# Kernel tuning notes

Measured on AMD Instinct MI355X. Metric: run time of the kernel, lower is better.

The kernel has to match this reference:

```python
import jax, jax.numpy as jnp
import numpy as np

NH = 16
HD = 128
ROPE_THETA = 10000.0


def _rope_tables(L, dtype):
    inv_freq = 1.0 / (ROPE_THETA ** (jnp.arange(0, HD, 2, dtype=jnp.float32) / HD))
    t = jnp.arange(L, dtype=jnp.float32)
    freqs = jnp.outer(t, inv_freq)          # [L, HD/2]
    emb = jnp.concatenate([freqs, freqs], axis=-1)  # [L, HD]
    return jnp.cos(emb).astype(dtype), jnp.sin(emb).astype(dtype)


def _rotate_half(x):
    x1, x2 = jnp.split(x, 2, axis=-1)
    return jnp.concatenate([-x2, x1], axis=-1)


def _apply_rope(x, cos, sin):
    return x * cos + _rotate_half(x) * sin


def setup_inputs() -> dict:
    key = jax.random.key(0)
    k1, k2, k3 = jax.random.split(key, 3)
    B, L, H = 2, 2048, 2048
    x = jax.random.normal(k1, (B, L, H), dtype=jnp.float32)
    w_qkv = jax.random.normal(k2, (3 * H, H), dtype=jnp.float32) * 0.02
    w_o = jax.random.normal(k3, (H, H), dtype=jnp.float32) * 0.02
    return {"x": x, "w_qkv": w_qkv, "w_o": w_o}


def reference(x, w_qkv, w_o):
    B, L, H = x.shape
    qkv = x @ w_qkv.T                                   # [B, L, 3H]
    qkv = qkv.reshape(B, L, 3, NH, HD).transpose(2, 0, 3, 1, 4)  # [3, B, NH, L, HD]
    q, k, v = qkv[0], qkv[1], qkv[2]
    cos, sin = _rope_tables(L, x.dtype)
    cos, sin = cos[None, None], sin[None, None]         # [1, 1, L, HD]
    q = _apply_rope(q, cos, sin)
    k = _apply_rope(k, cos, sin)
    scale = 1.0 / jnp.sqrt(jnp.asarray(HD, dtype=x.dtype))
    scores = jnp.einsum('bhqd,bhkd->bhqk', q, k) * scale
    causal = jnp.tril(jnp.ones((L, L), dtype=bool))
    scores = jnp.where(causal[None, None], scores, jnp.asarray(-1e30, dtype=x.dtype))
    attn = jax.nn.softmax(scores, axis=-1)
    out = jnp.einsum('bhqk,bhkd->bhqd', attn, v)        # [B, NH, L, HD]
    out = out.transpose(0, 2, 1, 3).reshape(B, L, H)
    return out @ w_o.T
```

## Files before the change

kernel.cpp:

```cpp
#include <hip/hip_runtime.h>

#define NHEADS 16
#define HD 128
#define LSEQ 2048
#define NBATCH 2
#define HDIM 2048
#define NQKV 6144
#define SCALE 0.08838834764831845f

typedef __attribute__((ext_vector_type(8))) short bfx8;
typedef __attribute__((ext_vector_type(4))) short bfx4;
typedef __attribute__((ext_vector_type(4))) float f32x4;

__device__ __forceinline__ unsigned short f2bf(float x) {
  unsigned u = __float_as_uint(x);
  u += 0x7fffu + ((u >> 16) & 1u);
  return (unsigned short)(u >> 16);
}
__device__ __forceinline__ float bf2f(unsigned short u) {
  return __uint_as_float(((unsigned)u) << 16);
}
__device__ __forceinline__ void gload_lds16(const void* g, void* l) {
  __builtin_amdgcn_global_load_lds(
      (const __attribute__((address_space(1))) unsigned int*)g,
      (__attribute__((address_space(3))) unsigned int*)l, 16, 0, 0);
}

__global__ __launch_bounds__(256) void cast_bf16_kernel(
    const float* __restrict__ in, unsigned short* __restrict__ out, int n4) {
  int i = blockIdx.x * 256 + threadIdx.x;
  if (i >= n4) return;
  float4 v = ((const float4*)in)[i];
  bfx4 o;
  o[0] = (short)f2bf(v.x);
  o[1] = (short)f2bf(v.y);
  o[2] = (short)f2bf(v.z);
  o[3] = (short)f2bf(v.w);
  ((bfx4*)out)[i] = o;
}

template<bool BF16OUT>
__global__ __launch_bounds__(256) void gemm_bt_kernel(
    const unsigned short* __restrict__ A, const unsigned short* __restrict__ B,
    void* __restrict__ Cout, int M, int N, int K) {
  __shared__ unsigned short lA[128 * 64];
  __shared__ unsigned short lB[128 * 64];
  const int tid = threadIdx.x;
  const int w = tid >> 6, lane = tid & 63;
  const int g = lane >> 4, ln = lane & 15;
  const int bm = blockIdx.x * 128, bn = blockIdx.y * 128;
  const int wm = (w >> 1) * 64, wn = (w & 1) * 64;
  const int srow = lane >> 3;
  const int scol = (lane & 7) * 8;

  f32x4 acc[4][4];
#pragma unroll
  for (int i = 0; i < 4; ++i)
#pragma unroll
    for (int j = 0; j < 4; ++j) acc[i][j] = (f32x4){0.f, 0.f, 0.f, 0.f};

  for (int k0 = 0; k0 < K; k0 += 64) {
#pragma unroll
    for (int p = 0; p < 4; ++p) {
      int seg = p * 4 + w;
      int row = seg * 8 + srow;
      const unsigned short* gA = A + (size_t)(bm + row) * K + (k0 + scol);
      const unsigned short* gB = B + (size_t)(bn + row) * K + (k0 + scol);
      gload_lds16(gA, lA + seg * 512);
      gload_lds16(gB, lB + seg * 512);
    }
    __syncthreads();
#pragma unroll
    for (int kk = 0; kk < 2; ++kk) {
      bfx8 af[4], bfr[4];
#pragma unroll
      for (int i = 0; i < 4; ++i)
        af[i] = *(const bfx8*)(lA + (wm + i * 16 + ln) * 64 + kk * 32 + g * 8);
#pragma unroll
      for (int j = 0; j < 4; ++j)
        bfr[j] = *(const bfx8*)(lB + (wn + j * 16 + ln) * 64 + kk * 32 + g * 8);
#pragma unroll
      for (int i = 0; i < 4; ++i)
#pragma unroll
        for (int j = 0; j < 4; ++j)
          acc[i][j] = __builtin_amdgcn_mfma_f32_16x16x32_bf16(af[i], bfr[j], acc[i][j], 0, 0, 0);
    }
    __syncthreads();
  }
#pragma unroll
  for (int i = 0; i < 4; ++i) {
    int row0 = bm + wm + i * 16 + g * 4;
#pragma unroll
    for (int j = 0; j < 4; ++j) {
      int col = bn + wn + j * 16 + ln;
#pragma unroll
      for (int r = 0; r < 4; ++r) {
        if constexpr (BF16OUT)
          ((unsigned short*)Cout)[(size_t)(row0 + r) * N + col] = f2bf(acc[i][j][r]);
        else
          ((float*)Cout)[(size_t)(row0 + r) * N + col] = acc[i][j][r];
      }
    }
  }
}

__global__ __launch_bounds__(256) void rope_scatter_kernel(
    const unsigned short* __restrict__ qkv,
    unsigned short* __restrict__ Qo, unsigned short* __restrict__ Ko,
    unsigned short* __restrict__ Vt) {
  __shared__ unsigned short lV[32 * 128];
  const int bh = blockIdx.x;
  const int l0 = blockIdx.y * 32;
  const int b = bh >> 4, h = bh & 15;
  const int tid = threadIdx.x;
#pragma unroll
  for (int it = 0; it < 2; ++it) {
    int idx = it * 256 + tid;
    int ll = idx >> 4;
    int dq = idx & 15;
    int l = l0 + ll;
    const unsigned short* row = qkv + (size_t)(b * LSEQ + l) * NQKV + h * HD;
    bfx4 qlo = *(const bfx4*)(row + dq * 4);
    bfx4 qhi = *(const bfx4*)(row + 64 + dq * 4);
    bfx4 klo = *(const bfx4*)(row + 2048 + dq * 4);
    bfx4 khi = *(const bfx4*)(row + 2048 + 64 + dq * 4);
    bfx4 vlo = *(const bfx4*)(row + 4096 + dq * 4);
    bfx4 vhi = *(const bfx4*)(row + 4096 + 64 + dq * 4);
    bfx4 oqlo, oqhi, oklo, okhi;
#pragma unroll
    for (int e = 0; e < 4; ++e) {
      int d2 = dq * 4 + e;
      float invf = exp2f(-(float)d2 * 0.2076205059304601f);
      float fr = (float)l * invf;
      float s, c;
      sincosf(fr, &s, &c);
      float xq1 = bf2f((unsigned short)qlo[e]), xq2 = bf2f((unsigned short)qhi[e]);
      oqlo[e] = (short)f2bf(xq1 * c - xq2 * s);
      oqhi[e] = (short)f2bf(xq2 * c + xq1 * s);
      float xk1 = bf2f((unsigned short)klo[e]), xk2 = bf2f((unsigned short)khi[e]);
      oklo[e] = (short)f2bf(xk1 * c - xk2 * s);
      okhi[e] = (short)f2bf(xk2 * c + xk1 * s);
    }
    size_t obase = ((size_t)bh * LSEQ + l) * HD;
    *(bfx4*)(Qo + obase + dq * 4) = oqlo;
    *(bfx4*)(Qo + obase + 64 + dq * 4) = oqhi;
    *(bfx4*)(Ko + obase + dq * 4) = oklo;
    *(bfx4*)(Ko + obase + 64 + dq * 4) = okhi;
    *(bfx4*)(lV + ll * 128 + dq * 4) = vlo;
    *(bfx4*)(lV + ll * 128 + 64 + dq * 4) = vhi;
  }
  __syncthreads();
#pragma unroll
  for (int it = 0; it < 16; ++it) {
    int idx = it * 256 + tid;
    int d = idx >> 5;
    int ll = idx & 31;
    Vt[((size_t)bh * HD + d) * LSEQ + l0 + ll] = lV[ll * 128 + d];
  }
}

__global__ __launch_bounds__(512, 4) void flash_kernel(
    const unsigned short* __restrict__ Q, const unsigned short* __restrict__ K,
    const unsigned short* __restrict__ Vt, unsigned short* __restrict__ O) {
  __shared__ unsigned short lKs[2][64 * 128];
  __shared__ unsigned short lVs[2][128 * 64];
  __shared__ unsigned short lP[8][16 * 40];
  const int bh = blockIdx.x;
  const int qt = 15 - (int)blockIdx.y;
  const int q0 = qt * 128;
  const int tid = threadIdx.x;
  const int w = tid >> 6, lane = tid & 63;
  const int g = lane >> 4, ln = lane & 15;
  const int q0w = q0 + w * 16;
  const unsigned short* Qb = Q + (size_t)bh * LSEQ * HD;
  const unsigned short* Kb = K + (size_t)bh * LSEQ * HD;
  const unsigned short* Vb = Vt + (size_t)bh * HD * LSEQ;
  unsigned short* Pw = lP[w];

  auto STAGE = [&](int buf, int kv0s) {
#pragma unroll
    for (int s = 0; s < 2; ++s) {
      int rl = s * 32 + w * 4 + (lane >> 4);
      int slot = lane & 15;
      const unsigned short* src =
          Kb + (size_t)(kv0s + rl) * HD + ((slot ^ (rl & 15)) * 8);
      gload_lds16(src, &lKs[buf][(s * 8192 + w * 1024) / 2]);
    }
#pragma unroll
    for (int s = 0; s < 2; ++s) {
      int d = s * 64 + w * 8 + (lane >> 3);
      int slot = lane & 7;
      const unsigned short* src =
          Vb + (size_t)d * LSEQ + kv0s + ((slot ^ (d & 7)) * 8);
      gload_lds16(src, &lVs[buf][(s * 8192 + w * 1024) / 2]);
    }
  };

  bfx8 qf[4];
#pragma unroll
  for (int c = 0; c < 4; ++c)
    qf[c] = *(const bfx8*)(Qb + (size_t)(q0w + ln) * HD + c * 32 + g * 8);

  f32x4 o[8];
#pragma unroll
  for (int dt = 0; dt < 8; ++dt) o[dt] = (f32x4){0.f, 0.f, 0.f, 0.f};
  float m = -1e30f, sum = 0.f;
  const int qg = q0w + ln;
  const int nch = 2 * qt + 2;

  STAGE(0, 0);
  __syncthreads();

  for (int ch = 0; ch < nch; ++ch) {
    const int kv0 = ch * 64;
    const int cur = ch & 1;
    if (ch + 1 < nch) STAGE(cur ^ 1, kv0 + 64);

    if (kv0 <= q0w + 15) {
      const char* lK0 = (const char*)lKs[cur];
      const char* lV0 = (const char*)lVs[cur];
      f32x4 s4[4];
#pragma unroll
      for (int kt = 0; kt < 4; ++kt) s4[kt] = (f32x4){0.f, 0.f, 0.f, 0.f};
#pragma unroll
      for (int c = 0; c < 4; ++c) {
        const int cbb = c * 64 + g * 16;
#pragma unroll
        for (int kt = 0; kt < 4; ++kt) {
          bfx8 kf = *(const bfx8*)(lK0 + (kt * 16 + ln) * 256 + (cbb ^ (ln << 4)));
          s4[kt] = __builtin_amdgcn_mfma_f32_16x16x32_bf16(kf, qf[c], s4[kt], 0, 0, 0);
        }
      }
      float tm = -1e30f;
      if (kv0 + 63 <= q0w) {
#pragma unroll
        for (int kt = 0; kt < 4; ++kt)
#pragma unroll
          for (int r = 0; r < 4; ++r) {
            s4[kt][r] *= SCALE;
            tm = fmaxf(tm, s4[kt][r]);
          }
      } else {
#pragma unroll
        for (int kt = 0; kt < 4; ++kt)
#pragma unroll
          for (int r = 0; r < 4; ++r) {
            int kvr = kv0 + kt * 16 + 4 * g + r;
            float v = (kvr <= qg) ? s4[kt][r] * SCALE : -1e30f;
            s4[kt][r] = v;
            tm = fmaxf(tm, v);
          }
      }
      tm = fmaxf(tm, __shfl_xor(tm, 16));
      tm = fmaxf(tm, __shfl_xor(tm, 32));
      float f = 1.f;
      const bool dorescale = !__all(tm <= m + 8.f);
      if (dorescale) {
        float mnew = fmaxf(m, tm);
        f = __expf(m - mnew);
        m = mnew;
      }
      float ts = 0.f;
      bfx4 pb4[4];
#pragma unroll
      for (int kt = 0; kt < 4; ++kt)
#pragma unroll
        for (int r = 0; r < 4; ++r) {
          float p = __expf(s4[kt][r] - m);
          ts += p;
          pb4[kt][r] = (short)f2bf(p);
        }
      ts += __shfl_xor(ts, 16);
      ts += __shfl_xor(ts, 32);
      sum = sum * f + ts;
      float fr0 = 1.f, fr1 = 1.f, fr2 = 1.f, fr3 = 1.f;
      if (dorescale) {
        fr0 = __shfl(f, 4 * g + 0);
        fr1 = __shfl(f, 4 * g + 1);
        fr2 = __shfl(f, 4 * g + 2);
        fr3 = __shfl(f, 4 * g + 3);
      }
#pragma unroll
      for (int kvh = 0; kvh < 2; ++kvh) {
        asm volatile("s_waitcnt lgkmcnt(0)" ::: "memory");
        __builtin_amdgcn_sched_barrier(0);
        *(bfx4*)(Pw + ln * 40 + 4 * g) = pb4[2 * kvh];
        *(bfx4*)(Pw + ln * 40 + 16 + 4 * g) = pb4[2 * kvh + 1];
        asm volatile("s_waitcnt lgkmcnt(0)" ::: "memory");
        __builtin_amdgcn_sched_barrier(0);
        bfx8 pf = *(const bfx8*)(Pw + ln * 40 + g * 8);
        if (kvh == 0 && dorescale) {
#pragma unroll
          for (int dt = 0; dt < 8; ++dt) {
            o[dt][0] *= fr0; o[dt][1] *= fr1; o[dt][2] *= fr2; o[dt][3] *= fr3;
          }
        }
#pragma unroll
        for (int dt = 0; dt < 8; ++dt) {
          bfx8 vf = *(const bfx8*)(lV0 + (dt * 16 + ln) * 128 +
                                   ((kvh * 64 + g * 16) ^ ((ln & 7) << 4)));
          o[dt] = __builtin_amdgcn_mfma_f32_16x16x32_bf16(pf, vf, o[dt], 0, 0, 0);
        }
      }
    }
    __syncthreads();
  }

  float inv = 1.f / sum;
  float ir0 = __shfl(inv, 4 * g + 0);
  float ir1 = __shfl(inv, 4 * g + 1);
  float ir2 = __shfl(inv, 4 * g + 2);
  float ir3 = __shfl(inv, 4 * g + 3);
  const int b = bh >> 4, h = bh & 15;
  unsigned short* Ob = O + (size_t)b * LSEQ * HDIM + h * HD;
#pragma unroll
  for (int dt = 0; dt < 8; ++dt) {
    Ob[(size_t)(q0w + 4 * g + 0) * HDIM + dt * 16 + ln] = f2bf(o[dt][0] * ir0);
    Ob[(size_t)(q0w + 4 * g + 1) * HDIM + dt * 16 + ln] = f2bf(o[dt][1] * ir1);
    Ob[(size_t)(q0w + 4 * g + 2) * HDIM + dt * 16 + ln] = f2bf(o[dt][2] * ir2);
    Ob[(size_t)(q0w + 4 * g + 3) * HDIM + dt * 16 + ln] = f2bf(o[dt][3] * ir3);
  }
}

extern "C" void kernel_launch(void* const* d_in, const int* in_sizes, int n_in,
                              void* d_out, int out_size, void* d_ws, size_t ws_size,
                              hipStream_t stream) {
  const float* x = (const float*)d_in[0];
  const float* w_qkv = (const float*)d_in[1];
  const float* w_o = (const float*)d_in[2];
  float* out = (float*)d_out;
  char* ws = (char*)d_ws;

  unsigned short* xb    = (unsigned short*)(ws + 0);
  unsigned short* wqkvb = (unsigned short*)(ws + 16777216);
  unsigned short* wob   = (unsigned short*)(ws + 41943040);
  unsigned short* qkvb  = (unsigned short*)(ws + 50331648);
  unsigned short* qb    = (unsigned short*)(ws + 100663296);
  unsigned short* kb    = (unsigned short*)(ws + 117440512);
  unsigned short* vtb   = (unsigned short*)(ws + 134217728);
  unsigned short* attnb = (unsigned short*)(ws + 0);

  cast_bf16_kernel<<<8388608 / 4 / 256, 256, 0, stream>>>(x, xb, 8388608 / 4);
  cast_bf16_kernel<<<12582912 / 4 / 256, 256, 0, stream>>>(w_qkv, wqkvb, 12582912 / 4);
  cast_bf16_kernel<<<4194304 / 4 / 256, 256, 0, stream>>>(w_o, wob, 4194304 / 4);

  gemm_bt_kernel<true><<<dim3(4096 / 128, 6144 / 128), 256, 0, stream>>>(
      xb, wqkvb, (void*)qkvb, 4096, 6144, 2048);

  rope_scatter_kernel<<<dim3(32, 64), 256, 0, stream>>>(qkvb, qb, kb, vtb);

  flash_kernel<<<dim3(32, 16), 512, 0, stream>>>(qb, kb, vtb, attnb);

  gemm_bt_kernel<false><<<dim3(4096 / 128, 2048 / 128), 256, 0, stream>>>(
      attnb, wob, (void*)out, 4096, 2048, 2048);
}
```

Baseline: 314.3 us.

## Add 256x256 double-buffered GEMM kernel with XCD swizzle for QKV projection

Adds a new bf16 GEMM kernel that uses 256x256 output tiles with 512 threads. It double-buffers LDS, loading the next K-slice through direct global-to-LDS copies with an XOR swizzle, and interleaves those loads with MFMA phases under a raised wave priority. Workgroup IDs are remapped so neighbouring tiles land on the same XCD. The QKV projection now uses this kernel to get more operand reuse and hide load latency. In exchange it needs 128 KB of LDS per block and carries high register pressure.

```diff
diff --git a/kernel.cpp b/kernel.cpp
--- a/kernel.cpp
+++ b/kernel.cpp
@@ -37,6 +37,102 @@
   o[2] = (short)f2bf(v.z);
   o[3] = (short)f2bf(v.w);
   ((bfx4*)out)[i] = o;
+}
+
+template<bool BF16OUT>
+__global__ __launch_bounds__(512, 2) void gemm256_kernel(
+    const unsigned short* __restrict__ A, const unsigned short* __restrict__ B,
+    void* __restrict__ Cout, int M, int N, int K) {
+  __shared__ unsigned short lA[2][256 * 64];
+  __shared__ unsigned short lB[2][256 * 64];
+  const int tid = threadIdx.x;
+  const int w = tid >> 6, lane = tid & 63;
+  const int g = lane >> 4, ln = lane & 15;
+  const int nmt = M >> 8, nnt = N >> 8;
+  const int nwg = nmt * nnt;
+  const int bid = blockIdx.x;
+  const int swz = (bid & 7) * (nwg >> 3) + (bid >> 3);
+  const int bm = (swz / nnt) * 256, bn = (swz % nnt) * 256;
+  const int wm = (w >> 2) * 128, wn = (w & 3) * 64;
+
+  auto STAGE = [&](int buf, int k0, int q) {
+    int rid = q * 64 + w * 8 + (lane >> 3);
+    int slot = lane & 7;
+    gload_lds16(A + (size_t)(bm + rid) * K + k0 + ((slot ^ (rid & 7)) << 3),
+                &lA[buf][(q * 512 + w * 64) * 8]);
+    gload_lds16(B + (size_t)(bn + rid) * K + k0 + ((slot ^ (rid & 7)) << 3),
+                &lB[buf][(q * 512 + w * 64) * 8]);
+  };
+
+  f32x4 acc[8][4];
+#pragma unroll
+  for (int i = 0; i < 8; ++i)
+#pragma unroll
+    for (int j = 0; j < 4; ++j) acc[i][j] = (f32x4){0.f, 0.f, 0.f, 0.f};
+
+#pragma unroll
+  for (int q = 0; q < 4; ++q) STAGE(0, 0, q);
+  asm volatile("s_waitcnt vmcnt(0)" ::: "memory");
+  asm volatile("s_barrier" ::: "memory");
+
+  const int nt = K >> 6;
+  for (int t = 0; t < nt; ++t) {
+    const int cur = t & 1;
+    const char* lAc = (const char*)lA[cur];
+    const char* lBc = (const char*)lB[cur];
+    const int k0n = (t + 1) << 6;
+    bfx8 bfrag[4][2];
+#pragma unroll
+    for (int ph = 0; ph < 4; ++ph) {
+      if (t + 1 < nt) STAGE(cur ^ 1, k0n, ph);
+      bfx8 afrag[2][2];
+#pragma unroll
+      for (int mi = 0; mi < 2; ++mi)
+#pragma unroll
+        for (int kk = 0; kk < 2; ++kk)
+          afrag[mi][kk] = *(const bfx8*)(lAc + (wm + ph * 32 + mi * 16 + ln) * 128 +
+                                         (((kk * 4 + g) ^ (ln & 7)) << 4));
+      if (ph == 0) {
+#pragma unroll
+        for (int nf = 0; nf < 4; ++nf)
+#pragma unroll
+          for (int kk = 0; kk < 2; ++kk)
+            bfrag[nf][kk] = *(const bfx8*)(lBc + (wn + nf * 16 + ln) * 128 +
+                                           (((kk * 4 + g) ^ (ln & 7)) << 4));
+      }
+      asm volatile("s_waitcnt lgkmcnt(0)" ::: "memory");
+      __builtin_amdgcn_sched_barrier(0);
+      __builtin_amdgcn_s_setprio(1);
+#pragma unroll
+      for (int kk = 0; kk < 2; ++kk)
+#pragma unroll
+        for (int mi = 0; mi < 2; ++mi)
+#pragma unroll
+          for (int nf = 0; nf < 4; ++nf)
+            acc[ph * 2 + mi][nf] = __builtin_amdgcn_mfma_f32_16x16x32_bf16(
+                afrag[mi][kk], bfrag[nf][kk], acc[ph * 2 + mi][nf], 0, 0, 0);
+      __builtin_amdgcn_s_setprio(0);
+      if (ph < 3) asm volatile("s_barrier" ::: "memory");
+    }
+    asm volatile("s_waitcnt vmcnt(0)" ::: "memory");
+    asm volatile("s_barrier" ::: "memory");
+  }
+
+#pragma unroll
+  for (int mf = 0; mf < 8; ++mf) {
+    int row0 = bm + wm + mf * 16 + g * 4;
+#pragma unroll
+    for (int nf = 0; nf < 4; ++nf) {
+      int col = bn + wn + nf * 16 + ln;
+#pragma unroll
+      for (int r = 0; r < 4; ++r) {
+        if constexpr (BF16OUT)
+          ((unsigned short*)Cout)[(size_t)(row0 + r) * N + col] = f2bf(acc[mf][nf][r]);
+        else
+          ((float*)Cout)[(size_t)(row0 + r) * N + col] = acc[mf][nf][r];
+      }
+    }
+  }
 }
 
 template<bool BF16OUT>
@@ -344,7 +440,7 @@
   cast_bf16_kernel<<<12582912 / 4 / 256, 256, 0, stream>>>(w_qkv, wqkvb, 12582912 / 4);
   cast_bf16_kernel<<<4194304 / 4 / 256, 256, 0, stream>>>(w_o, wob, 4194304 / 4);
 
-  gemm_bt_kernel<true><<<dim3(4096 / 128, 6144 / 128), 256, 0, stream>>>(
+  gemm256_kernel<true><<<(4096 / 256) * (6144 / 256), 512, 0, stream>>>(
       xb, wqkvb, (void*)qkvb, 4096, 6144, 2048);
 
   rope_scatter_kernel<<<dim3(32, 64), 256, 0, stream>>>(qkvb, qb, kb, vtb);
```

Measured after the change: 354.7 us. 12.9% more time.

## Replace LDS-staged GEMM with direct global-to-register MFMA loads and swizzled tiles

Applied to the files above, without the earlier changes.

The GEMM kernel no longer stages A/B tiles through shared memory with global_load_lds and barriers. Each wave now loads its MFMA fragments straight from global memory into registers. Blocks are launched on a 1D grid with an XCD-style swizzle of block index to tile, and the QKV projection uses a 128x192 tile. This removes the LDS traffic and __syncthreads stalls, but each row is now fetched redundantly by several waves through L2/L1. Loads are also strided and not coalesced per lane, and with no software prefetch, latency may be exposed.

```diff
diff --git a/kernel.cpp b/kernel.cpp
--- a/kernel.cpp
+++ b/kernel.cpp
@@ -39,66 +39,65 @@
   ((bfx4*)out)[i] = o;
 }
 
-template<bool BF16OUT>
-__global__ __launch_bounds__(256) void gemm_bt_kernel(
+template<int WN, bool BF16OUT>
+__global__ __launch_bounds__(256, 2) void gemm_flat_kernel(
     const unsigned short* __restrict__ A, const unsigned short* __restrict__ B,
     void* __restrict__ Cout, int M, int N, int K) {
-  __shared__ unsigned short lA[128 * 64];
-  __shared__ unsigned short lB[128 * 64];
+  constexpr int NF = WN / 16;
+  constexpr int BN = 2 * WN;
   const int tid = threadIdx.x;
   const int w = tid >> 6, lane = tid & 63;
   const int g = lane >> 4, ln = lane & 15;
-  const int bm = blockIdx.x * 128, bn = blockIdx.y * 128;
-  const int wm = (w >> 1) * 64, wn = (w & 1) * 64;
-  const int srow = lane >> 3;
-  const int scol = (lane & 7) * 8;
-
-  f32x4 acc[4][4];
+  const int nnt = N / BN;
+  const int nwg = (M >> 7) * nnt;
+  const int bid = blockIdx.x;
+  const int swz = (bid & 7) * (nwg >> 3) + (bid >> 3);
+  const int bm = (swz / nnt) * 128, bn = (swz % nnt) * BN;
+  const int rowA = bm + (w >> 1) * 64 + ln;
+  const int colB = bn + (w & 1) * WN + ln;
+  const unsigned short* pA = A + (size_t)rowA * K + g * 8;
+  const unsigned short* pB = B + (size_t)colB * K + g * 8;
+
+  f32x4 acc[4][NF];
 #pragma unroll
   for (int i = 0; i < 4; ++i)
 #pragma unroll
-    for (int j = 0; j < 4; ++j) acc[i][j] = (f32x4){0.f, 0.f, 0.f, 0.f};
+    for (int j = 0; j < NF; ++j) acc[i][j] = (f32x4){0.f, 0.f, 0.f, 0.f};
 
   for (int k0 = 0; k0 < K; k0 += 64) {
-#pragma unroll
-    for (int p = 0; p < 4; ++p) {
-      int seg = p * 4 + w;
-      int row = seg * 8 + srow;
-      const unsigned short* gA = A + (size_t)(bm + row) * K + (k0 + scol);
-      const unsigned short* gB = B + (size_t)(bn + row) * K + (k0 + scol);
-      gload_lds16(gA, lA + seg * 512);
-      gload_lds16(gB, lB + seg * 512);
-    }
-    __syncthreads();
-#pragma unroll
-    for (int kk = 0; kk < 2; ++kk) {
-      bfx8 af[4], bfr[4];
-#pragma unroll
-      for (int i = 0; i < 4; ++i)
-        af[i] = *(const bfx8*)(lA + (wm + i * 16 + ln) * 64 + kk * 32 + g * 8);
-#pragma unroll
-      for (int j = 0; j < 4; ++j)
-        bfr[j] = *(const bfx8*)(lB + (wn + j * 16 + ln) * 64 + kk * 32 + g * 8);
-#pragma unroll
-      for (int i = 0; i < 4; ++i)
-#pragma unroll
-        for (int j = 0; j < 4; ++j)
-          acc[i][j] = __builtin_amdgcn_mfma_f32_16x16x32_bf16(af[i], bfr[j], acc[i][j], 0, 0, 0);
-    }
-    __syncthreads();
-  }
-#pragma unroll
-  for (int i = 0; i < 4; ++i) {
-    int row0 = bm + wm + i * 16 + g * 4;
-#pragma unroll
-    for (int j = 0; j < 4; ++j) {
-      int col = bn + wn + j * 16 + ln;
+    bfx8 a[4][2], b[NF][2];
+#pragma unroll
+    for (int mf = 0; mf < 4; ++mf)
+#pragma unroll
+      for (int kk = 0; kk < 2; ++kk)
+        a[mf][kk] = *(const bfx8*)(pA + (size_t)mf * 16 * K + k0 + kk * 32);
+#pragma unroll
+    for (int nf = 0; nf < NF; ++nf)
+#pragma unroll
+      for (int kk = 0; kk < 2; ++kk)
+        b[nf][kk] = *(const bfx8*)(pB + (size_t)nf * 16 * K + k0 + kk * 32);
+#pragma unroll
+    for (int kk = 0; kk < 2; ++kk)
+#pragma unroll
+      for (int mf = 0; mf < 4; ++mf)
+#pragma unroll
+        for (int nf = 0; nf < NF; ++nf)
+          acc[mf][nf] = __builtin_amdgcn_mfma_f32_16x16x32_bf16(
+              a[mf][kk], b[nf][kk], acc[mf][nf], 0, 0, 0);
+  }
+
+#pragma unroll
+  for (int mf = 0; mf < 4; ++mf) {
+    int row0 = bm + (w >> 1) * 64 + mf * 16 + g * 4;
+#pragma unroll
+    for (int nf = 0; nf < NF; ++nf) {
+      int col = bn + (w & 1) * WN + nf * 16 + ln;
 #pragma unroll
       for (int r = 0; r < 4; ++r) {
         if constexpr (BF16OUT)
-          ((unsigned short*)Cout)[(size_t)(row0 + r) * N + col] = f2bf(acc[i][j][r]);
+          ((unsigned short*)Cout)[(size_t)(row0 + r) * N + col] = f2bf(acc[mf][nf][r]);
         else
-          ((float*)Cout)[(size_t)(row0 + r) * N + col] = acc[i][j][r];
+          ((float*)Cout)[(size_t)(row0 + r) * N + col] = acc[mf][nf][r];
       }
     }
   }
@@ -344,13 +343,13 @@
   cast_bf16_kernel<<<12582912 / 4 / 256, 256, 0, stream>>>(w_qkv, wqkvb, 12582912 / 4);
   cast_bf16_kernel<<<4194304 / 4 / 256, 256, 0, stream>>>(w_o, wob, 4194304 / 4);
 
-  gemm_bt_kernel<true><<<dim3(4096 / 128, 6144 / 128), 256, 0, stream>>>(
+  gemm_flat_kernel<96, true><<<(4096 / 128) * (6144 / 192), 256, 0, stream>>>(
       xb, wqkvb, (void*)qkvb, 4096, 6144, 2048);
 
   rope_scatter_kernel<<<dim3(32, 64), 256, 0, stream>>>(qkvb, qb, kb, vtb);
 
   flash_kernel<<<dim3(32, 16), 512, 0, stream>>>(qb, kb, vtb, attnb);
 
-  gemm_bt_kernel<false><<<dim3(4096 / 128, 2048 / 128), 256, 0, stream>>>(
+  gemm_flat_kernel<64, false><<<(4096 / 128) * (2048 / 128), 256, 0, stream>>>(
       attnb, wob, (void*)out, 4096, 2048, 2048);
 }
```

After: 558.9 us. 77.8% more time.
